# Optimization experiments

Hardware: AMD Instinct MI355X
Metric: run time of the kernel (lower is better)

The kernel has to match this reference:

```python
import jax, jax.numpy as jnp
import numpy as np

N_EXPERT = 8
TOP_K = 2
NEG_INF = -1e9  # finite sentinel so softmax grads stay well-defined


def setup_inputs() -> dict:
    key = jax.random.key(0)
    ks = jax.random.split(key, 8)
    B, S, D, F, E = 2, 2048, 1024, 4096, N_EXPERT
    sd = 1.0 / np.sqrt(D)
    sf = 1.0 / np.sqrt(F)
    return {
        "x": jax.random.normal(ks[0], (B, S, D), jnp.float32),
        "noise": jax.random.normal(ks[1], (B, S, E), jnp.float32),
        "Wr": jax.random.normal(ks[2], (D, E), jnp.float32) * sd,
        "br": jnp.zeros((E,), jnp.float32),
        "Wn": jax.random.normal(ks[3], (D, E), jnp.float32) * sd,
        "bn": jnp.zeros((E,), jnp.float32),
        "W1": jax.random.normal(ks[4], (E, D, F), jnp.float32) * sd,
        "b1": jnp.zeros((E, F), jnp.float32),
        "W2": jax.random.normal(ks[5], (E, F, D), jnp.float32) * sf,
        "b2": jnp.zeros((E, D), jnp.float32),
    }


def reference(x, noise, Wr, br, Wn, bn, W1, b1, W2, b2):
    # NoisyTopkRouter: logits + noise * softplus(noise_logits)
    logits = jnp.einsum("bsd,de->bse", x, Wr) + br
    noise_logits = jnp.einsum("bsd,de->bse", x, Wn) + bn
    noisy = logits + noise * jax.nn.softplus(noise_logits)

    # keep only top-k logits, -inf elsewhere, softmax over experts
    _, top_ids = jax.lax.top_k(noisy, TOP_K)                  # [B,S,K]
    sel = jnp.sum(jax.nn.one_hot(top_ids, N_EXPERT, dtype=noisy.dtype), axis=-2) > 0  # [B,S,E]
    gates = jax.nn.softmax(jnp.where(sel, noisy, NEG_INF), axis=-1)  # zeros off top-k

    # Expert MLP: Linear -> ReLU -> Linear (dropout = 0 at inference).
    # Gates are exactly zero for non-selected experts, so the dense einsum
    # combine equals the original masked gather/scatter-add.
    h = jax.nn.relu(jnp.einsum("bsd,edf->ebsf", x, W1) + b1[:, None, None, :])
    eo = jnp.einsum("ebsf,efd->ebsd", h, W2) + b2[:, None, None, :]
    return jnp.einsum("bse,ebsd->bsd", gates, eo)
```

## Files before the change

### kernel.cpp

```cpp
#include <hip/hip_runtime.h>

#define T_TOK 4096
#define DDIM 1024
#define FDIM 4096
#define NE 8
#define NPAIR 8192
#define MAXT128 72

typedef short bf16x8 __attribute__((ext_vector_type(8)));
typedef float f32x4 __attribute__((ext_vector_type(4)));

__device__ inline unsigned short f2bf(float f) {
  union { float f; unsigned u; } a; a.f = f;
  unsigned r = a.u + 0x7fffu + ((a.u >> 16) & 1u);
  return (unsigned short)(r >> 16);
}

__device__ __forceinline__ void gload16(const void* g, void* l) {
  __builtin_amdgcn_global_load_lds(
      (const __attribute__((address_space(1))) unsigned int*)g,
      (__attribute__((address_space(3))) unsigned int*)l, 16, 0, 0);
}

__global__ __launch_bounds__(256) void router_kernel(
    const float* __restrict__ x, const float* __restrict__ noise,
    const float* __restrict__ Wr, const float* __restrict__ br,
    const float* __restrict__ Wn, const float* __restrict__ bn,
    int* __restrict__ tok_top, float* __restrict__ tok_gate,
    ushort* __restrict__ xb)
{
  int t = blockIdx.x * 4 + (threadIdx.x >> 6);
  int lane = threadIdx.x & 63;
  const float* xr = x + (size_t)t * DDIM;
  ushort* xo = xb + (size_t)t * DDIM;
  float accR[NE] = {}, accN[NE] = {};
  for (int d = lane; d < DDIM; d += 64) {
    float xv = xr[d];
    xo[d] = f2bf(xv);
    const float* wr = Wr + (size_t)d * NE;
    const float* wn = Wn + (size_t)d * NE;
#pragma unroll
    for (int e = 0; e < NE; ++e) {
      accR[e] = fmaf(xv, wr[e], accR[e]);
      accN[e] = fmaf(xv, wn[e], accN[e]);
    }
  }
#pragma unroll
  for (int off = 32; off > 0; off >>= 1) {
#pragma unroll
    for (int e = 0; e < NE; ++e) {
      accR[e] += __shfl_xor(accR[e], off);
      accN[e] += __shfl_xor(accN[e], off);
    }
  }
  if (lane == 0) {
    float noisy[NE];
#pragma unroll
    for (int e = 0; e < NE; ++e) {
      float lg = accR[e] + br[e];
      float nl = accN[e] + bn[e];
      float sp = fmaxf(nl, 0.f) + log1pf(expf(-fabsf(nl)));
      noisy[e] = lg + noise[(size_t)t * NE + e] * sp;
    }
    int e0 = 0;
#pragma unroll
    for (int e = 1; e < NE; ++e) if (noisy[e] > noisy[e0]) e0 = e;
    int e1 = (e0 == 0) ? 1 : 0;
#pragma unroll
    for (int e = 0; e < NE; ++e)
      if (e != e0 && e != e1 && noisy[e] > noisy[e1]) e1 = e;
    float v0 = noisy[e0], v1 = noisy[e1];
    float ex = __expf(v1 - v0);
    float inv = 1.f / (1.f + ex);
    tok_top[t * 2] = e0; tok_top[t * 2 + 1] = e1;
    tok_gate[t * 2] = inv; tok_gate[t * 2 + 1] = ex * inv;
  }
}

__global__ __launch_bounds__(256) void scan_scatter_kernel(
    const int* __restrict__ tok_top, int* __restrict__ off, int* __restrict__ tiles,
    int* __restrict__ pair_tok, int* __restrict__ tok_ppos)
{
  __shared__ int smat[NE][256];
  __shared__ int tot[NE];
  __shared__ int loff[NE];
  int tid = threadIdx.x;
  int c[NE] = {};
  for (int i = 0; i < 16; ++i) {
    int t = tid * 16 + i;
    int e0 = tok_top[2 * t], e1 = tok_top[2 * t + 1];
#pragma unroll
    for (int e = 0; e < NE; ++e) c[e] += (e0 == e) + (e1 == e);
  }
#pragma unroll
  for (int e = 0; e < NE; ++e) smat[e][tid] = c[e];
  __syncthreads();
  {
    int ge = tid >> 5;
    int gl = tid & 31;
    int vals[8], s = 0;
#pragma unroll
    for (int j = 0; j < 8; ++j) { vals[j] = smat[ge][gl * 8 + j]; s += vals[j]; }
    int incl = s;
#pragma unroll
    for (int d = 1; d < 32; d <<= 1) {
      int o = __shfl_up(incl, d);
      if (gl >= d) incl += o;
    }
    int run = incl - s;
#pragma unroll
    for (int j = 0; j < 8; ++j) { smat[ge][gl * 8 + j] = run; run += vals[j]; }
    if (gl == 31) tot[ge] = incl;
  }
  __syncthreads();
  if (tid == 0) {
    int s = 0, nt = 0;
    for (int e = 0; e < NE; ++e) {
      loff[e] = s; off[e] = s;
      int tt = (tot[e] + 127) >> 7;
      for (int m = 0; m < tt; ++m) tiles[1 + nt++] = (e << 8) | m;
      s += tot[e];
    }
    off[NE] = s;
    tiles[0] = nt;
  }
  __syncthreads();
  for (int i = 0; i < 16; ++i) {
    int t = tid * 16 + i;
#pragma unroll
    for (int k = 0; k < 2; ++k) {
      int e = tok_top[2 * t + k];
      int pos = loff[e] + smat[e][tid];
      smat[e][tid] = smat[e][tid] + 1;
      pair_tok[pos] = t;
      tok_ppos[2 * t + k] = pos;
    }
  }
}

__global__ __launch_bounds__(256) void transpose_w1_kernel(
    const float* __restrict__ W1, ushort* __restrict__ WT1)
{
  __shared__ float tile[64][65];
  int z = blockIdx.z;
  const float* src = W1 + (size_t)z * DDIM * FDIM;
  ushort* dst = WT1 + (size_t)z * FDIM * DDIM;
  int c0 = blockIdx.x * 64, r0 = blockIdx.y * 64;
  int tid = threadIdx.x;
  int tr = tid >> 4;
  int tc4 = (tid & 15) * 4;
#pragma unroll
  for (int i = 0; i < 64; i += 16) {
    float4 v = *(const float4*)(src + (size_t)(r0 + tr + i) * FDIM + c0 + tc4);
    tile[tr + i][tc4] = v.x; tile[tr + i][tc4 + 1] = v.y;
    tile[tr + i][tc4 + 2] = v.z; tile[tr + i][tc4 + 3] = v.w;
  }
  __syncthreads();
  int cc = tid >> 4;
  int rr4 = (tid & 15) * 4;
#pragma unroll
  for (int i = 0; i < 64; i += 16) {
    int c = cc + i;
    ushort4 o;
    o.x = f2bf(tile[rr4][c]); o.y = f2bf(tile[rr4 + 1][c]);
    o.z = f2bf(tile[rr4 + 2][c]); o.w = f2bf(tile[rr4 + 3][c]);
    *(ushort4*)(dst + (size_t)(c0 + c) * DDIM + r0 + rr4) = o;
  }
}

template<int KD, int ND, int EPI, int INDIR, int TFUSE>
__global__ __launch_bounds__(256) void gemm4_kernel(
    const ushort* __restrict__ A, const ushort* __restrict__ BT,
    const int* __restrict__ off, const int* __restrict__ tiles,
    const int* __restrict__ pair_tok, const float* __restrict__ bias,
    ushort* __restrict__ Hout, float* __restrict__ EOout,
    const float* __restrict__ W2src, ushort* __restrict__ WT2dst)
{
  constexpr int GX = ND / 128;
  constexpr int NKT = KD / 64;
  __shared__ __align__(16) ushort As[128 * 64];
  __shared__ __align__(16) ushort Bs[128 * 64];

  int total = tiles[0] * GX;
  int orig = blockIdx.x + GX * (int)blockIdx.y;
  if (orig >= total) {
    if constexpr (TFUSE) {
      int idx = orig - total;
      if (idx >= NE * (FDIM / 64) * (DDIM / 64)) return;
      __shared__ float ttile[64][65];
      int e2 = idx >> 10;
      int rem = idx & 1023;
      int ft = rem >> 4, dt = rem & 15;
      const float* src = W2src + (size_t)e2 * FDIM * DDIM;
      ushort* dst = WT2dst + (size_t)e2 * DDIM * FDIM;
      int r0 = ft * 64, c0 = dt * 64;
      int tid2 = threadIdx.x;
      int tr = tid2 >> 4;
      int tc4 = (tid2 & 15) * 4;
#pragma unroll
      for (int i = 0; i < 64; i += 16) {
        float4 v = *(const float4*)(src + (size_t)(r0 + tr + i) * DDIM + c0 + tc4);
        ttile[tr + i][tc4] = v.x; ttile[tr + i][tc4 + 1] = v.y;
        ttile[tr + i][tc4 + 2] = v.z; ttile[tr + i][tc4 + 3] = v.w;
      }
      __syncthreads();
      int cc = tid2 >> 4;
      int rr4 = (tid2 & 15) * 4;
#pragma unroll
      for (int i = 0; i < 64; i += 16) {
        int c = cc + i;
        ushort4 o;
        o.x = f2bf(ttile[rr4][c]); o.y = f2bf(ttile[rr4 + 1][c]);
        o.z = f2bf(ttile[rr4 + 2][c]); o.w = f2bf(ttile[rr4 + 3][c]);
        *(ushort4*)(dst + (size_t)(c0 + c) * FDIM + r0 + rr4) = o;
      }
    }
    return;
  }
  int q = total >> 3, r = total & 7, xcd = orig & 7, idx = orig >> 3;
  int wg = (xcd < r ? xcd * (q + 1) : r * (q + 1) + (xcd - r) * q) + idx;
  int ti = wg / GX, bx = wg - ti * GX;

  int te = tiles[1 + ti];
  int e = te >> 8, mt = te & 255;
  int base = off[e];
  int cnt = off[e + 1] - base;
  int m0 = mt << 7, n0 = bx << 7;

  int tid = threadIdx.x, lane = tid & 63, wid = tid >> 6;
  int wr = wid >> 1, wc = wid & 1;

  int arow[4];
#pragma unroll
  for (int c = 0; c < 4; ++c) {
    int rl = (c * 256 + tid) >> 3;
    int mr = m0 + rl; if (mr >= cnt) mr = cnt - 1;
    arow[c] = INDIR ? pair_tok[base + mr] : base + mr;
  }
  const char* Ab = (const char*)A;
  const char* Bgb = (const char*)(BT + ((size_t)e * ND + n0) * KD);

  f32x4 acc[4][4] = {};

  for (int t = 0; t < NKT; ++t) {
    __syncthreads();
    int kb = t * 128;
#pragma unroll
    for (int c = 0; c < 4; ++c) {
      int ch = c * 256 + tid;
      int row = ch >> 3, b = (ch & 7) * 16;
      gload16(Ab + (size_t)arow[c] * (KD * 2) + kb + (b ^ ((row & 7) << 4)),
              (char*)As + ch * 16);
    }
#pragma unroll
    for (int c = 0; c < 4; ++c) {
      int ch = c * 256 + tid;
      int row = ch >> 3, b = (ch & 7) * 16;
      gload16(Bgb + (size_t)row * (KD * 2) + kb + (b ^ ((row & 7) << 4)),
              (char*)Bs + ch * 16);
    }
    __syncthreads();

    bf16x8 af[4][2], bv[4][2];
#pragma unroll
    for (int m = 0; m < 4; ++m) {
      int row = wr * 64 + m * 16 + (lane & 15);
      int sw = (row & 7) << 4;
#pragma unroll
      for (int ks = 0; ks < 2; ++ks)
        af[m][ks] = *(const bf16x8*)((const char*)As + row * 128 +
                                     ((ks * 64 + (lane >> 4) * 16) ^ sw));
    }
#pragma unroll
    for (int n = 0; n < 4; ++n) {
      int row = wc * 64 + n * 16 + (lane & 15);
      int sw = (row & 7) << 4;
#pragma unroll
      for (int ks = 0; ks < 2; ++ks)
        bv[n][ks] = *(const bf16x8*)((const char*)Bs + row * 128 +
                                     ((ks * 64 + (lane >> 4) * 16) ^ sw));
    }
#pragma unroll
    for (int ks = 0; ks < 2; ++ks)
#pragma unroll
      for (int m = 0; m < 4; ++m)
#pragma unroll
        for (int n = 0; n < 4; ++n)
          acc[m][n] = __builtin_amdgcn_mfma_f32_16x16x32_bf16(
              af[m][ks], bv[n][ks], acc[m][n], 0, 0, 0);
  }

  float bvv[4];
#pragma unroll
  for (int n = 0; n < 4; ++n)
    bvv[n] = bias[(size_t)e * ND + n0 + wc * 64 + n * 16 + (lane & 15)];
  int rq = (lane >> 4) << 2;
#pragma unroll
  for (int m = 0; m < 4; ++m) {
#pragma unroll
    for (int qq = 0; qq < 4; ++qq) {
      int rr = m0 + wr * 64 + m * 16 + rq + qq;
      if (rr < cnt) {
#pragma unroll
        for (int n = 0; n < 4; ++n) {
          int col = n0 + wc * 64 + n * 16 + (lane & 15);
          float v = acc[m][n][qq] + bvv[n];
          if (EPI == 0) {
            v = fmaxf(v, 0.f);
            Hout[(size_t)(base + rr) * ND + col] = f2bf(v);
          } else {
            EOout[(size_t)(base + rr) * ND + col] = v;
          }
        }
      }
    }
  }
}

__global__ __launch_bounds__(256) void combine_kernel(
    const float* __restrict__ eo, const int* __restrict__ tok_ppos,
    const float* __restrict__ tok_gate, float* __restrict__ out)
{
  int t = blockIdx.x;
  int tid = threadIdx.x;
  int p0 = tok_ppos[t * 2], p1 = tok_ppos[t * 2 + 1];
  float g0 = tok_gate[t * 2], g1 = tok_gate[t * 2 + 1];
  float4 a = ((const float4*)(eo + (size_t)p0 * DDIM))[tid];
  float4 b = ((const float4*)(eo + (size_t)p1 * DDIM))[tid];
  float4 o;
  o.x = g0 * a.x + g1 * b.x;
  o.y = g0 * a.y + g1 * b.y;
  o.z = g0 * a.z + g1 * b.z;
  o.w = g0 * a.w + g1 * b.w;
  ((float4*)(out + (size_t)t * DDIM))[tid] = o;
}

extern "C" void kernel_launch(void* const* d_in, const int* in_sizes, int n_in,
                              void* d_out, int out_size, void* d_ws, size_t ws_size,
                              hipStream_t stream)
{
  const float* x     = (const float*)d_in[0];
  const float* noise = (const float*)d_in[1];
  const float* Wr    = (const float*)d_in[2];
  const float* br    = (const float*)d_in[3];
  const float* Wn    = (const float*)d_in[4];
  const float* bn    = (const float*)d_in[5];
  const float* W1    = (const float*)d_in[6];
  const float* b1    = (const float*)d_in[7];
  const float* W2    = (const float*)d_in[8];
  const float* b2    = (const float*)d_in[9];
  float* out = (float*)d_out;

  char* ws = (char*)d_ws;
  size_t o = 0;
  auto alloc = [&](size_t sz) {
    void* p = ws + o;
    o = (o + sz + 255) & ~(size_t)255;
    return p;
  };
  ushort* WT1 = (ushort*)alloc((size_t)NE * FDIM * DDIM * 2);
  ushort* WT2 = (ushort*)alloc((size_t)NE * DDIM * FDIM * 2);
  ushort* XB  = (ushort*)alloc((size_t)T_TOK * DDIM * 2);
  ushort* H   = (ushort*)alloc((size_t)(NPAIR + 256) * FDIM * 2);
  float*  EO  = (float*)alloc((size_t)(NPAIR + 256) * DDIM * 4);
  int*    TOK_TOP  = (int*)alloc(T_TOK * 2 * 4);
  float*  TOK_GATE = (float*)alloc(T_TOK * 2 * 4);
  int*    TOK_PPOS = (int*)alloc(T_TOK * 2 * 4);
  int*    PAIR_TOK = (int*)alloc((NPAIR + 256) * 4);
  int*    OFF = (int*)alloc(64);
  int*    TILES = (int*)alloc((1 + MAXT128) * 4);

  router_kernel<<<T_TOK / 4, 256, 0, stream>>>(x, noise, Wr, br, Wn, bn,
                                               TOK_TOP, TOK_GATE, XB);
  scan_scatter_kernel<<<1, 256, 0, stream>>>(TOK_TOP, OFF, TILES, PAIR_TOK, TOK_PPOS);
  transpose_w1_kernel<<<dim3(64, 16, 8), 256, 0, stream>>>(W1, WT1);
  gemm4_kernel<DDIM, FDIM, 0, 1, 1>
      <<<dim3(FDIM / 128, 328), 256, 0, stream>>>(XB, WT1, OFF, TILES, PAIR_TOK, b1, H,
                                                  nullptr, W2, WT2);
  gemm4_kernel<FDIM, DDIM, 1, 0, 0>
      <<<dim3(DDIM / 128, MAXT128), 256, 0, stream>>>(H, WT2, OFF, TILES, PAIR_TOK, b2,
                                                      nullptr, EO, nullptr, nullptr);
  combine_kernel<<<T_TOK, 256, 0, stream>>>(EO, TOK_PPOS, TOK_GATE, out);
}
```

Before: 318.9 us.

## Use 256x256 ping-pong 8-wave GEMM for first expert layer with grid-stride W2 transpose

Replaces the first expert GEMM (X·W1) with a new 512-thread kernel that uses 256x256 output tiles, double-buffered 64KB LDS stages, direct global-to-LDS loads, swizzled LDS reads and a phased MFMA schedule with priority hints. The scan kernel now also emits a 256-row tile list. The fused W2 transpose in spare blocks becomes grid-stride, with two tiles per block, and both transposes write 16-byte vectors. The goal is higher MFMA utilisation and less operand traffic per FLOP. In exchange it needs 128KB of LDS per block and wastes more work on padding rows in partially filled 256-row tiles.

Result: no change. 313.9 us (-1.6%).

```diff
diff --git a/kernel.cpp b/kernel.cpp
--- a/kernel.cpp
+++ b/kernel.cpp
@@ -6,6 +6,7 @@
 #define NE 8
 #define NPAIR 8192
 #define MAXT128 72
+#define MAXT256 48
 
 typedef short bf16x8 __attribute__((ext_vector_type(8)));
 typedef float f32x4 __attribute__((ext_vector_type(4)));
@@ -78,7 +79,8 @@
 }
 
 __global__ __launch_bounds__(256) void scan_scatter_kernel(
-    const int* __restrict__ tok_top, int* __restrict__ off, int* __restrict__ tiles,
+    const int* __restrict__ tok_top, int* __restrict__ off,
+    int* __restrict__ tiles128, int* __restrict__ tiles256,
     int* __restrict__ pair_tok, int* __restrict__ tok_ppos)
 {
   __shared__ int smat[NE][256];
@@ -114,15 +116,18 @@
   }
   __syncthreads();
   if (tid == 0) {
-    int s = 0, nt = 0;
+    int s = 0, nt1 = 0, nt2 = 0;
     for (int e = 0; e < NE; ++e) {
       loff[e] = s; off[e] = s;
-      int tt = (tot[e] + 127) >> 7;
-      for (int m = 0; m < tt; ++m) tiles[1 + nt++] = (e << 8) | m;
+      int t1 = (tot[e] + 127) >> 7;
+      for (int m = 0; m < t1; ++m) tiles128[1 + nt1++] = (e << 8) | m;
+      int t2 = (tot[e] + 255) >> 8;
+      for (int m = 0; m < t2; ++m) tiles256[1 + nt2++] = (e << 8) | m;
       s += tot[e];
     }
     off[NE] = s;
-    tiles[0] = nt;
+    tiles128[0] = nt1;
+    tiles256[0] = nt2;
   }
   __syncthreads();
   for (int i = 0; i < 16; ++i) {
@@ -156,67 +161,233 @@
     tile[tr + i][tc4 + 2] = v.z; tile[tr + i][tc4 + 3] = v.w;
   }
   __syncthreads();
-  int cc = tid >> 4;
-  int rr4 = (tid & 15) * 4;
-#pragma unroll
-  for (int i = 0; i < 64; i += 16) {
-    int c = cc + i;
-    ushort4 o;
-    o.x = f2bf(tile[rr4][c]); o.y = f2bf(tile[rr4 + 1][c]);
-    o.z = f2bf(tile[rr4 + 2][c]); o.w = f2bf(tile[rr4 + 3][c]);
-    *(ushort4*)(dst + (size_t)(c0 + c) * DDIM + r0 + rr4) = o;
-  }
-}
-
-template<int KD, int ND, int EPI, int INDIR, int TFUSE>
-__global__ __launch_bounds__(256) void gemm4_kernel(
+  int rr = (tid & 7) * 8;
+  int cbase = tid >> 3;
+#pragma unroll
+  for (int cc = 0; cc < 64; cc += 32) {
+    int c = cbase + cc;
+    ushort tmp[8];
+#pragma unroll
+    for (int j = 0; j < 8; ++j) tmp[j] = f2bf(tile[rr + j][c]);
+    *(uint4*)(dst + (size_t)(c0 + c) * DDIM + r0 + rr) = *(uint4*)tmp;
+  }
+}
+
+template<int KD, int ND, int INDIR>
+__global__ __launch_bounds__(512) void gemm8p_kernel(
     const ushort* __restrict__ A, const ushort* __restrict__ BT,
     const int* __restrict__ off, const int* __restrict__ tiles,
     const int* __restrict__ pair_tok, const float* __restrict__ bias,
-    ushort* __restrict__ Hout, float* __restrict__ EOout,
+    ushort* __restrict__ Hout,
     const float* __restrict__ W2src, ushort* __restrict__ WT2dst)
 {
-  constexpr int GX = ND / 128;
+  constexpr int GX = ND / 256;
   constexpr int NKT = KD / 64;
-  __shared__ __align__(16) ushort As[128 * 64];
-  __shared__ __align__(16) ushort Bs[128 * 64];
+  constexpr int NIT = NKT / 2;
+  __shared__ __align__(16) char lds[2 * 65536];
 
   int total = tiles[0] * GX;
   int orig = blockIdx.x + GX * (int)blockIdx.y;
   if (orig >= total) {
-    if constexpr (TFUSE) {
-      int idx = orig - total;
-      if (idx >= NE * (FDIM / 64) * (DDIM / 64)) return;
-      __shared__ float ttile[64][65];
+    int S = GX * (int)gridDim.y - total;
+    int half = threadIdx.x >> 8;
+    int tid2 = threadIdx.x & 255;
+    float (*tt)[65] = (float(*)[65])(lds + half * 16704);
+    int tr = tid2 >> 4, tc4 = (tid2 & 15) * 4;
+    int rr = (tid2 & 7) * 8, cbase = tid2 >> 3;
+    for (int j = orig - total; j < 4096; j += S) {
+      int idx = 2 * j + half;
       int e2 = idx >> 10;
       int rem = idx & 1023;
       int ft = rem >> 4, dt = rem & 15;
       const float* src = W2src + (size_t)e2 * FDIM * DDIM;
       ushort* dst = WT2dst + (size_t)e2 * DDIM * FDIM;
       int r0 = ft * 64, c0 = dt * 64;
-      int tid2 = threadIdx.x;
-      int tr = tid2 >> 4;
-      int tc4 = (tid2 & 15) * 4;
 #pragma unroll
       for (int i = 0; i < 64; i += 16) {
         float4 v = *(const float4*)(src + (size_t)(r0 + tr + i) * DDIM + c0 + tc4);
-        ttile[tr + i][tc4] = v.x; ttile[tr + i][tc4 + 1] = v.y;
-        ttile[tr + i][tc4 + 2] = v.z; ttile[tr + i][tc4 + 3] = v.w;
+        tt[tr + i][tc4] = v.x; tt[tr + i][tc4 + 1] = v.y;
+        tt[tr + i][tc4 + 2] = v.z; tt[tr + i][tc4 + 3] = v.w;
       }
       __syncthreads();
-      int cc = tid2 >> 4;
-      int rr4 = (tid2 & 15) * 4;
-#pragma unroll
-      for (int i = 0; i < 64; i += 16) {
-        int c = cc + i;
-        ushort4 o;
-        o.x = f2bf(ttile[rr4][c]); o.y = f2bf(ttile[rr4 + 1][c]);
-        o.z = f2bf(ttile[rr4 + 2][c]); o.w = f2bf(ttile[rr4 + 3][c]);
-        *(ushort4*)(dst + (size_t)(c0 + c) * FDIM + r0 + rr4) = o;
+#pragma unroll
+      for (int cc = 0; cc < 64; cc += 32) {
+        int c = cbase + cc;
+        ushort tmp[8];
+#pragma unroll
+        for (int jj = 0; jj < 8; ++jj) tmp[jj] = f2bf(tt[rr + jj][c]);
+        *(uint4*)(dst + (size_t)(c0 + c) * FDIM + r0 + rr) = *(uint4*)tmp;
       }
+      __syncthreads();
     }
     return;
   }
+  int q = total >> 3, r = total & 7, xcd = orig & 7, idx = orig >> 3;
+  int wg = (xcd < r ? xcd * (q + 1) : r * (q + 1) + (xcd - r) * q) + idx;
+  int ti = wg / GX, bx = wg - ti * GX;
+
+  int te = tiles[1 + ti];
+  int e = te >> 8, mt = te & 255;
+  int base = off[e];
+  int cnt = off[e + 1] - base;
+  int m0 = mt << 8, n0 = bx << 8;
+
+  int tid = threadIdx.x, lane = tid & 63, wid = tid >> 6;
+  int wr = wid >> 2, wc = wid & 3;
+  int lr = lane & 15, hi = lane >> 4;
+  int swl = (lane & 7) << 4;
+  int wrOff = wr * 16384;
+  int wcLow = wc & 1;
+  int wcHiOff = (wc >> 1) * 16384;
+
+  const char* aptr[2][2];
+  const char* bptr[2][2];
+  {
+    const char* Ab = (const char*)A;
+    const char* Bb = (const char*)(BT + ((size_t)e * ND + n0) * KD);
+#pragma unroll
+    for (int h = 0; h < 2; ++h)
+#pragma unroll
+      for (int c = 0; c < 2; ++c) {
+        int ch = c * 512 + tid;
+        int rl = ch >> 3;
+        int sc = ((ch & 7) * 16) ^ ((rl & 7) << 4);
+        int mr = m0 + h * 128 + rl; if (mr >= cnt) mr = cnt - 1;
+        int ar = INDIR ? pair_tok[base + mr] : base + mr;
+        aptr[h][c] = Ab + (size_t)ar * (KD * 2) + sc;
+        bptr[h][c] = Bb + (size_t)(h * 128 + rl) * (KD * 2) + sc;
+      }
+  }
+
+#define SH_A(T, H)                                                        \
+  if ((T) < NKT) {                                                        \
+    char* d_ = lds + ((T) & 1) * 65536 + (H) * 16384 + tid * 16;          \
+    gload16(aptr[H][0] + (T) * 128, d_);                                  \
+    gload16(aptr[H][1] + (T) * 128, d_ + 8192);                           \
+  }
+#define SH_B(T, H)                                                        \
+  if ((T) < NKT) {                                                        \
+    char* d_ = lds + ((T) & 1) * 65536 + 32768 + (H) * 16384 + tid * 16;  \
+    gload16(bptr[H][0] + (T) * 128, d_);                                  \
+    gload16(bptr[H][1] + (T) * 128, d_ + 8192);                           \
+  }
+#define LDA(MH, BUF)                                                      \
+  { _Pragma("unroll") for (int mm = 0; mm < 4; ++mm) {                    \
+      int rr_ = (MH) * 64 + mm * 16 + lr;                                 \
+      _Pragma("unroll") for (int ks = 0; ks < 2; ++ks)                    \
+        af[mm][ks] = *(const bf16x8*)((BUF) + wrOff + rr_ * 128 +         \
+                                      ((ks * 64 + hi * 16) ^ swl)); } }
+#define LDB(NH, BUF, BV)                                                  \
+  { _Pragma("unroll") for (int nn = 0; nn < 2; ++nn) {                    \
+      int rr_ = wcLow * 64 + (NH) * 32 + nn * 16 + lr;                    \
+      _Pragma("unroll") for (int ks = 0; ks < 2; ++ks)                    \
+        BV[nn][ks] = *(const bf16x8*)((BUF) + 32768 + wcHiOff + rr_ * 128 + \
+                                      ((ks * 64 + hi * 16) ^ swl)); } }
+#define MMA(MH, NH, BV)                                                   \
+  { _Pragma("unroll") for (int ks = 0; ks < 2; ++ks)                      \
+    _Pragma("unroll") for (int mm = 0; mm < 4; ++mm)                      \
+    _Pragma("unroll") for (int nn = 0; nn < 2; ++nn)                      \
+      acc[(MH) * 4 + mm][(NH) * 2 + nn] =                                 \
+        __builtin_amdgcn_mfma_f32_16x16x32_bf16(                          \
+          af[mm][ks], BV[nn][ks], acc[(MH) * 4 + mm][(NH) * 2 + nn], 0, 0, 0); }
+#define PH_MID                                                            \
+  __builtin_amdgcn_sched_barrier(0);                                      \
+  __builtin_amdgcn_s_barrier();                                           \
+  asm volatile("s_waitcnt lgkmcnt(0)" ::: "memory");                      \
+  __builtin_amdgcn_sched_barrier(0);                                      \
+  __builtin_amdgcn_s_setprio(1);
+#define PH_END                                                            \
+  __builtin_amdgcn_s_setprio(0);                                          \
+  __builtin_amdgcn_sched_barrier(0);                                      \
+  __builtin_amdgcn_s_barrier();
+
+  f32x4 acc[8][4] = {};
+  bf16x8 af[4][2], bv0[2][2], bv1[2][2];
+
+  SH_A(0, 0); SH_A(0, 1); SH_B(0, 0); SH_B(0, 1); SH_B(1, 0); SH_B(1, 1);
+  asm volatile("s_waitcnt vmcnt(4)" ::: "memory");
+  __builtin_amdgcn_sched_barrier(0);
+  __builtin_amdgcn_s_barrier();
+
+  const char* buf0 = lds;
+  const char* buf1 = lds + 65536;
+
+  for (int it = 0; it < NIT; ++it) {
+    int t0 = 2 * it, t1 = t0 + 1;
+    LDA(0, buf0); LDB(0, buf0, bv0);
+    SH_A(t1, 0);
+    PH_MID; MMA(0, 0, bv0); PH_END;
+    LDB(1, buf0, bv1);
+    SH_A(t1, 1);
+    PH_MID; MMA(0, 1, bv1); PH_END;
+    LDA(1, buf0);
+    SH_B(t0 + 2, 0);
+    PH_MID; MMA(1, 1, bv1); PH_END;
+    SH_A(t0 + 2, 0);
+    PH_MID; MMA(1, 0, bv0);
+    __builtin_amdgcn_s_setprio(0);
+    if (t0 + 2 < NKT) asm volatile("s_waitcnt vmcnt(4)" ::: "memory");
+    else              asm volatile("s_waitcnt vmcnt(0)" ::: "memory");
+    __builtin_amdgcn_sched_barrier(0);
+    __builtin_amdgcn_s_barrier();
+    LDA(0, buf1); LDB(0, buf1, bv0);
+    SH_A(t0 + 2, 1);
+    PH_MID; MMA(0, 0, bv0); PH_END;
+    LDB(1, buf1, bv1);
+    SH_B(t0 + 2, 1);
+    PH_MID; MMA(0, 1, bv1); PH_END;
+    LDA(1, buf1);
+    SH_B(t1 + 2, 0);
+    PH_MID; MMA(1, 1, bv1); PH_END;
+    SH_B(t1 + 2, 1);
+    PH_MID; MMA(1, 0, bv0);
+    __builtin_amdgcn_s_setprio(0);
+    if (t1 + 2 < NKT) asm volatile("s_waitcnt vmcnt(4)" ::: "memory");
+    else              asm volatile("s_waitcnt vmcnt(0)" ::: "memory");
+    __builtin_amdgcn_sched_barrier(0);
+    __builtin_amdgcn_s_barrier();
+  }
+
+  int rq = hi << 2;
+#pragma unroll
+  for (int m = 0; m < 8; ++m) {
+#pragma unroll
+    for (int qq = 0; qq < 4; ++qq) {
+      int rr2 = m0 + wr * 128 + m * 16 + rq + qq;
+      if (rr2 < cnt) {
+#pragma unroll
+        for (int n = 0; n < 4; ++n) {
+          int col = n0 + wc * 64 + n * 16 + lr;
+          float v = fmaxf(acc[m][n][qq] + bias[(size_t)e * ND + col], 0.f);
+          Hout[(size_t)(base + rr2) * ND + col] = f2bf(v);
+        }
+      }
+    }
+  }
+#undef SH_A
+#undef SH_B
+#undef LDA
+#undef LDB
+#undef MMA
+#undef PH_MID
+#undef PH_END
+}
+
+template<int KD, int ND, int EPI, int INDIR>
+__global__ __launch_bounds__(256) void gemm4_kernel(
+    const ushort* __restrict__ A, const ushort* __restrict__ BT,
+    const int* __restrict__ off, const int* __restrict__ tiles,
+    const int* __restrict__ pair_tok, const float* __restrict__ bias,
+    ushort* __restrict__ Hout, float* __restrict__ EOout)
+{
+  constexpr int GX = ND / 128;
+  constexpr int NKT = KD / 64;
+  __shared__ __align__(16) ushort As[128 * 64];
+  __shared__ __align__(16) ushort Bs[128 * 64];
+
+  int total = tiles[0] * GX;
+  int orig = blockIdx.x + GX * (int)blockIdx.y;
+  if (orig >= total) return;
   int q = total >> 3, r = total & 7, xcd = orig & 7, idx = orig >> 3;
   int wg = (xcd < r ? xcd * (q + 1) : r * (q + 1) + (xcd - r) * q) + idx;
   int ti = wg / GX, bx = wg - ti * GX;
@@ -368,17 +539,19 @@
   int*    TOK_PPOS = (int*)alloc(T_TOK * 2 * 4);
   int*    PAIR_TOK = (int*)alloc((NPAIR + 256) * 4);
   int*    OFF = (int*)alloc(64);
-  int*    TILES = (int*)alloc((1 + MAXT128) * 4);
+  int*    TILES128 = (int*)alloc((1 + MAXT128) * 4);
+  int*    TILES256 = (int*)alloc((1 + MAXT256) * 4);
 
   router_kernel<<<T_TOK / 4, 256, 0, stream>>>(x, noise, Wr, br, Wn, bn,
                                                TOK_TOP, TOK_GATE, XB);
-  scan_scatter_kernel<<<1, 256, 0, stream>>>(TOK_TOP, OFF, TILES, PAIR_TOK, TOK_PPOS);
+  scan_scatter_kernel<<<1, 256, 0, stream>>>(TOK_TOP, OFF, TILES128, TILES256,
+                                             PAIR_TOK, TOK_PPOS);
   transpose_w1_kernel<<<dim3(64, 16, 8), 256, 0, stream>>>(W1, WT1);
-  gemm4_kernel<DDIM, FDIM, 0, 1, 1>
-      <<<dim3(FDIM / 128, 328), 256, 0, stream>>>(XB, WT1, OFF, TILES, PAIR_TOK, b1, H,
-                                                  nullptr, W2, WT2);
-  gemm4_kernel<FDIM, DDIM, 1, 0, 0>
-      <<<dim3(DDIM / 128, MAXT128), 256, 0, stream>>>(H, WT2, OFF, TILES, PAIR_TOK, b2,
-                                                      nullptr, EO, nullptr, nullptr);
+  gemm8p_kernel<DDIM, FDIM, 1>
+      <<<dim3(FDIM / 256, MAXT256), 512, 0, stream>>>(XB, WT1, OFF, TILES256, PAIR_TOK,
+                                                      b1, H, W2, WT2);
+  gemm4_kernel<FDIM, DDIM, 1, 0>
+      <<<dim3(DDIM / 128, MAXT128), 256, 0, stream>>>(H, WT2, OFF, TILES128, PAIR_TOK,
+                                                      b2, nullptr, EO);
   combine_kernel<<<T_TOK, 256, 0, stream>>>(EO, TOK_PPOS, TOK_GATE, out);
 }
```
